# Optimization experiments

Hardware: AMD Instinct MI355X
Metric: run time of the kernel (lower is better)

Reference implementation:

```python
import jax, jax.numpy as jnp
import numpy as np

B, S, IN_DIM, OUT_DIM = 16, 1024, 1024, 1024
NEG_SLOPE = 0.01  # torch F.leaky_relu default


def setup_inputs() -> dict:
    key = jax.random.key(0)
    ks = jax.random.split(key, 10)
    sc_in = 1.0 / np.sqrt(IN_DIM)
    sc_out = 1.0 / np.sqrt(OUT_DIM)
    return {
        "xs": jax.random.normal(ks[0], (B, S, IN_DIM), dtype=jnp.float32),
        "mask": jax.random.randint(ks[1], (B, S), 0, 2, dtype=jnp.int32),
        "Wk": jax.random.uniform(ks[2], (OUT_DIM, IN_DIM), jnp.float32, -sc_in, sc_in),
        "bk": jax.random.uniform(ks[3], (OUT_DIM,), jnp.float32, -sc_in, sc_in),
        "Wq": jax.random.uniform(ks[4], (OUT_DIM, IN_DIM), jnp.float32, -sc_in, sc_in),
        "bq": jax.random.uniform(ks[5], (OUT_DIM,), jnp.float32, -sc_in, sc_in),
        "Wv": jax.random.uniform(ks[6], (OUT_DIM, IN_DIM), jnp.float32, -sc_in, sc_in),
        "bv": jax.random.uniform(ks[7], (OUT_DIM,), jnp.float32, -sc_in, sc_in),
        "Wlin": jax.random.uniform(ks[8], (OUT_DIM, OUT_DIM), jnp.float32, -sc_out, sc_out),
        "blin": jax.random.uniform(ks[9], (OUT_DIM,), jnp.float32, -sc_out, sc_out),
    }


def reference(xs, mask, Wk, bk, Wq, bq, Wv, bv, Wlin, blin):
    # projections: torch Linear is x @ W.T + b
    K = jnp.einsum('bsi,oi->bso', xs, Wk) + bk  # [B,S,D]
    Q = jnp.einsum('bsi,oi->bso', xs, Wq) + bq  # [B,S,D]
    V = jnp.einsum('bsi,oi->bso', xs, Wv) + bv  # [B,S,D]
    # qk[b,s,e] = sum_d K[b,s,d] * Q[b,e,d]
    qk = jnp.einsum('bsd,bed->bse', K, Q) / xs.shape[-1]
    # mask.repeat(1,S).view(B,S,S) => element [b,i,j] = mask[b,j] (column/key mask)
    qk = jnp.where(mask[:, None, :].astype(bool), qk, -jnp.inf)
    a = jax.nn.softmax(qk, axis=-1)  # [B,S,S]
    # faithful to einsum('bij,bik->bik'): sum a over last axis, scale V elementwise
    attn = jnp.sum(a, axis=-1, keepdims=True) * V  # [B,S,D]
    out = jnp.einsum('bsd,od->bso', attn, Wlin) + blin
    return jnp.where(out >= 0, out, NEG_SLOPE * out)
```

## Files before the change

kernel.cpp:

```cpp
#include <hip/hip_runtime.h>
#include <hip/hip_bf16.h>
#include <stdint.h>


#define M_TOT 16384
#define KDIM  1024
#define NDIM  1024
#define NKT   32

typedef __attribute__((ext_vector_type(8))) short bf16x8;
typedef __attribute__((ext_vector_type(4))) float f32x4;
typedef __attribute__((ext_vector_type(4))) unsigned short u16x4;
typedef __attribute__((ext_vector_type(8))) unsigned short u16x8;

static __device__ __forceinline__ unsigned short f2bf(float f) {
    union { float f; unsigned int u; } v; v.f = f;
    unsigned int u = v.u;
    return (unsigned short)((u + 0x7fffu + ((u >> 16) & 1u)) >> 16);
}

static __device__ __forceinline__ u16x8 pack8(float4 a, float4 b) {
    u16x8 p = { f2bf(a.x), f2bf(a.y), f2bf(a.z), f2bf(a.w),
                f2bf(b.x), f2bf(b.y), f2bf(b.z), f2bf(b.w) };
    return p;
}

static __device__ __forceinline__ void gload16(const void* g, void* l) {
    __builtin_amdgcn_global_load_lds(
        (__attribute__((address_space(1))) void*)(g),
        (__attribute__((address_space(3))) void*)(l), 16, 0, 0);
}

static __device__ __forceinline__ int swz128(int p) {
    return p ^ (((p >> 7) & 7) << 4);
}

__global__ __launch_bounds__(256) void prep0x_kernel(
    const float* __restrict__ Wv, const float* __restrict__ Wlin,
    const float* __restrict__ bv, const float* __restrict__ blin,
    const float* __restrict__ xs, unsigned short* __restrict__ Wvt,
    unsigned short* __restrict__ Wlb, float* __restrict__ bcomb,
    unsigned short* __restrict__ Xb) {
    __shared__ float Tl[64 * 65];
    const int bid = blockIdx.x;
    const int t = threadIdx.x;

    if (bid >= 768) {
        const size_t base = (((size_t)(bid - 768)) * 256 + t) * 8;
        #pragma unroll
        for (int itr = 0; itr < 4; ++itr) {
            const size_t idx = base + (size_t)itr * (size_t)(2048 * 256 * 8);
            float4 a = *(const float4*)&xs[idx];
            float4 b = *(const float4*)&xs[idx + 4];
            *(u16x8*)&Xb[idx] = pack8(a, b);
        }
        return;
    }

    if (bid < 256) {
        const int dt = bid >> 4;
        const int it = bid & 15;
        const int r = t >> 2;
        const int c0 = (t & 3) * 16;
        #pragma unroll
        for (int u = 0; u < 4; ++u) {
            float4 v = *(const float4*)&Wv[((size_t)(dt * 64 + r)) * NDIM + it * 64 + c0 + 4 * u];
            Tl[r * 65 + c0 + 4 * u + 0] = v.x;
            Tl[r * 65 + c0 + 4 * u + 1] = v.y;
            Tl[r * 65 + c0 + 4 * u + 2] = v.z;
            Tl[r * 65 + c0 + 4 * u + 3] = v.w;
        }
        __syncthreads();
        const int i = t >> 2;
        const int dq = (t & 3) * 16;
        float v[16];
        #pragma unroll
        for (int u = 0; u < 16; ++u) v[u] = Tl[(dq + u) * 65 + i];
        u16x8 p0 = { f2bf(v[0]), f2bf(v[1]), f2bf(v[2]), f2bf(v[3]),
                     f2bf(v[4]), f2bf(v[5]), f2bf(v[6]), f2bf(v[7]) };
        u16x8 p1 = { f2bf(v[8]), f2bf(v[9]), f2bf(v[10]), f2bf(v[11]),
                     f2bf(v[12]), f2bf(v[13]), f2bf(v[14]), f2bf(v[15]) };
        unsigned short* dst = &Wvt[((size_t)(it * 64 + i)) * KDIM + dt * 64 + dq];
        *(u16x8*)dst = p0;
        *(u16x8*)(dst + 8) = p1;
    } else if (bid < 512) {
        const size_t idx = (((size_t)(bid - 256)) * 256 + t) * 16;
        float4 a = *(const float4*)&Wlin[idx];
        float4 b = *(const float4*)&Wlin[idx + 4];
        float4 c = *(const float4*)&Wlin[idx + 8];
        float4 d = *(const float4*)&Wlin[idx + 12];
        *(u16x8*)&Wlb[idx] = pack8(a, b);
        *(u16x8*)&Wlb[idx + 8] = pack8(c, d);
    } else {
        const int wave = t >> 6, lane = t & 63;
        const int o = (bid - 512) * 4 + wave;
        float s = 0.f;
        for (int d = lane; d < KDIM; d += 64) s += Wlin[o * KDIM + d] * bv[d];
        #pragma unroll
        for (int off = 32; off > 0; off >>= 1) s += __shfl_down(s, off, 64);
        if (lane == 0) bcomb[o] = s + blin[o];
    }
}

__global__ __launch_bounds__(256) void wcomb_kernel(
    const unsigned short* __restrict__ Wlb, const unsigned short* __restrict__ Wvt,
    unsigned short* __restrict__ Wc) {
    __shared__ unsigned short As[64 * 32];
    __shared__ unsigned short Bs[64 * 32];
    const int t = threadIdx.x;
    const int ot = blockIdx.x >> 4;
    const int it = blockIdx.x & 15;
    const int w = t >> 6, l = t & 63;
    const int wr = (w >> 1) * 32, wc = (w & 1) * 32;
    const int lr = l & 15, lk = l >> 4;

    f32x4 acc[2][2] = {};

    const unsigned short* gA = &Wlb[((size_t)(ot * 64 + (t >> 2))) * KDIM + (t & 3) * 8];
    const unsigned short* gB = &Wvt[((size_t)(it * 64 + (t >> 2))) * KDIM + (t & 3) * 8];
    unsigned short* lA = &As[w * 512];
    unsigned short* lB = &Bs[w * 512];

    for (int kt = 0; kt < KDIM / 32; ++kt) {
        gload16(gA + kt * 32, lA);
        gload16(gB + kt * 32, lB);
        __syncthreads();
        bf16x8 af[2], bfr[2];
        #pragma unroll
        for (int fi = 0; fi < 2; ++fi)
            af[fi] = *(bf16x8*)&As[(wr + fi * 16 + lr) * 32 + lk * 8];
        #pragma unroll
        for (int fj = 0; fj < 2; ++fj)
            bfr[fj] = *(bf16x8*)&Bs[(wc + fj * 16 + lr) * 32 + lk * 8];
        #pragma unroll
        for (int fi = 0; fi < 2; ++fi)
            #pragma unroll
            for (int fj = 0; fj < 2; ++fj)
                acc[fi][fj] = __builtin_amdgcn_mfma_f32_16x16x32_bf16(
                    af[fi], bfr[fj], acc[fi][fj], 0, 0, 0);
        __syncthreads();
    }
    #pragma unroll
    for (int fi = 0; fi < 2; ++fi)
        #pragma unroll
        for (int fj = 0; fj < 2; ++fj)
            #pragma unroll
            for (int r = 0; r < 4; ++r) {
                const int o = ot * 64 + wr + fi * 16 + lk * 4 + r;
                const int i = it * 64 + wc + fj * 16 + lr;
                Wc[(size_t)o * KDIM + i] = f2bf(acc[fi][fj][r]);
            }
}

__global__ __launch_bounds__(512, 4) void main_mb(
    const unsigned short* __restrict__ Xb, const unsigned short* __restrict__ Wc,
    const float* __restrict__ bcomb, float* __restrict__ out) {
    extern __shared__ char lds[];
    const int tid = threadIdx.x;
    const int w = tid >> 6, l = tid & 63;
    const int wm = w >> 1, wn = w & 1;
    const int lr = l & 15, lk = l >> 4;

    const int swzb = ((blockIdx.x & 7) << 6) | (blockIdx.x >> 3);
    const int mt = swzb >> 3, nt = swzb & 7;

    int aoff[4], boff[4];
    #pragma unroll
    for (int fi = 0; fi < 4; ++fi) {
        const int r = wm * 64 + fi * 16 + lr;
        aoff[fi] = swz128(((r >> 1) << 7) | ((r & 1) << 6) | (lk << 4));
    }
    #pragma unroll
    for (int fj = 0; fj < 4; ++fj) {
        const int r = wn * 64 + fj * 16 + lr;
        boff[fj] = 16384 + swz128(((r >> 1) << 7) | ((r & 1) << 6) | (lk << 4));
    }

    const char* srcA[2];
    #pragma unroll
    for (int c = 0; c < 2; ++c) {
        const int q = c * 8192 + tid * 16;
        const int p = swz128(q);
        const int r = ((p >> 7) << 1) | ((p >> 6) & 1);
        srcA[c] = (const char*)Xb + ((size_t)(mt * 256 + r)) * 2048 + (p & 63);
    }
    const char* srcB;
    {
        const int q = tid * 16;
        const int p = swz128(q);
        const int r = ((p >> 7) << 1) | ((p >> 6) & 1);
        srcB = (const char*)Wc + ((size_t)(nt * 128 + r)) * 2048 + (p & 63);
    }
    const int ldsAw = w * 1024;
    const int ldsBw = 16384 + w * 1024;

    f32x4 acc[4][4] = {};

#define STAGE(TT, BUF)                                                         \
    do {                                                                       \
        gload16(srcA[0] + (size_t)(TT) * 64, (BUF) + ldsAw);                   \
        gload16(srcA[1] + (size_t)(TT) * 64, (BUF) + 8192 + ldsAw);            \
        gload16(srcB + (size_t)(TT) * 64, (BUF) + ldsBw);                      \
    } while (0)

    STAGE(0, lds);

    for (int kt = 0; kt < NKT; ++kt) {
        char* cbuf = lds + (kt & 1) * 24576;
        char* nbuf = lds + ((kt & 1) ^ 1) * 24576;

        if (kt < NKT - 1) {
            STAGE(kt + 1, nbuf);
            asm volatile("s_waitcnt vmcnt(3)" ::: "memory");
        } else {
            asm volatile("s_waitcnt vmcnt(0)" ::: "memory");
        }
        __builtin_amdgcn_s_barrier();

        bf16x8 af[4], bfr[4];
        #pragma unroll
        for (int fi = 0; fi < 4; ++fi)
            af[fi] = *(const bf16x8*)(cbuf + aoff[fi]);
        #pragma unroll
        for (int fj = 0; fj < 4; ++fj)
            bfr[fj] = *(const bf16x8*)(cbuf + boff[fj]);

        __builtin_amdgcn_s_setprio(1);
        #pragma unroll
        for (int fi = 0; fi < 4; ++fi)
            #pragma unroll
            for (int fj = 0; fj < 4; ++fj)
                acc[fi][fj] = __builtin_amdgcn_mfma_f32_16x16x32_bf16(
                    af[fi], bfr[fj], acc[fi][fj], 0, 0, 0);
        __builtin_amdgcn_s_setprio(0);

        __builtin_amdgcn_s_barrier();
    }
#undef STAGE

    #pragma unroll
    for (int fi = 0; fi < 4; ++fi)
        #pragma unroll
        for (int fj = 0; fj < 4; ++fj) {
            const int col = nt * 128 + wn * 64 + fj * 16 + lr;
            const float b = bcomb[col];
            #pragma unroll
            for (int r = 0; r < 4; ++r) {
                const int row = mt * 256 + wm * 64 + fi * 16 + lk * 4 + r;
                float v = acc[fi][fj][r] + b;
                out[(size_t)row * NDIM + col] = v >= 0.f ? v : 0.01f * v;
            }
        }
}

__global__ __launch_bounds__(256) void main_gemm_f32(
    const float* __restrict__ X, const unsigned short* __restrict__ Wc,
    const float* __restrict__ bcomb, float* __restrict__ out) {
    __shared__ unsigned short As[128 * 32];
    __shared__ unsigned short Bs[128 * 32];
    const int t = threadIdx.x;
    const int nt = blockIdx.x & 7;
    const int mt = blockIdx.x >> 3;
    const int w = t >> 6, l = t & 63;
    const int wr = (w >> 1) * 64, wcc = (w & 1) * 64;
    const int lr = l & 15, lk = l >> 4;

    f32x4 acc[4][4] = {};

    const int arow = t >> 3;
    const int akq = t & 7;
    const int brow = t >> 2;
    const int bc4 = t & 3;

    for (int kt = 0; kt < KDIM / 32; ++kt) {
        float4 av[4];
        #pragma unroll
        for (int j = 0; j < 4; ++j) {
            const int row = j * 32 + arow;
            av[j] = *(const float4*)&X[(mt * 128 + row) * KDIM + kt * 32 + akq * 4];
        }
        __syncthreads();
        #pragma unroll
        for (int j = 0; j < 4; ++j) {
            const int row = j * 32 + arow;
            u16x4 p = { f2bf(av[j].x), f2bf(av[j].y), f2bf(av[j].z), f2bf(av[j].w) };
            *(u16x4*)&As[row * 32 + akq * 4] = p;
        }
        #pragma unroll
        for (int j = 0; j < 2; ++j) {
            const int row = j * 64 + brow;
            const unsigned short* g = &Wc[(nt * 128 + row) * KDIM + kt * 32 + bc4 * 8];
            unsigned short* ldst = &Bs[(j * 256 + w * 64) * 8];
            gload16(g, ldst);
        }
        __syncthreads();
        bf16x8 af[4], bfr[4];
        #pragma unroll
        for (int fi = 0; fi < 4; ++fi)
            af[fi] = *(bf16x8*)&As[(wr + fi * 16 + lr) * 32 + lk * 8];
        #pragma unroll
        for (int fj = 0; fj < 4; ++fj)
            bfr[fj] = *(bf16x8*)&Bs[(wcc + fj * 16 + lr) * 32 + lk * 8];
        #pragma unroll
        for (int fi = 0; fi < 4; ++fi)
            #pragma unroll
            for (int fj = 0; fj < 4; ++fj)
                acc[fi][fj] = __builtin_amdgcn_mfma_f32_16x16x32_bf16(
                    af[fi], bfr[fj], acc[fi][fj], 0, 0, 0);
    }

    #pragma unroll
    for (int fi = 0; fi < 4; ++fi)
        #pragma unroll
        for (int fj = 0; fj < 4; ++fj) {
            const int col = nt * 128 + wcc + fj * 16 + lr;
            const float b = bcomb[col];
            #pragma unroll
            for (int r = 0; r < 4; ++r) {
                const int row = mt * 128 + wr + fi * 16 + lk * 4 + r;
                float v = acc[fi][fj][r] + b;
                out[row * NDIM + col] = v >= 0.f ? v : 0.01f * v;
            }
        }
}

extern "C" void kernel_launch(void* const* d_in, const int* in_sizes, int n_in,
                              void* d_out, int out_size, void* d_ws, size_t ws_size,
                              hipStream_t stream) {
    const float* xs   = (const float*)d_in[0];
    const float* Wv   = (const float*)d_in[6];
    const float* bv   = (const float*)d_in[7];
    const float* Wlin = (const float*)d_in[8];
    const float* blin = (const float*)d_in[9];

    unsigned short* Wc = (unsigned short*)d_ws;
    float* bcomb = (float*)((char*)d_ws + 2097152);
    unsigned short* Xb = (unsigned short*)((char*)d_ws + 2101248);
    float* out = (float*)d_out;

    unsigned short* Wvt = (unsigned short*)d_out;
    unsigned short* Wlb = (unsigned short*)((char*)d_out + 2097152);

    const size_t NEED = 2101248 + (size_t)M_TOT * KDIM * 2;
    if (ws_size >= NEED) {
        (void)hipFuncSetAttribute((const void*)main_mb,
                                  hipFuncAttributeMaxDynamicSharedMemorySize,
                                  49152);
        hipLaunchKernelGGL(prep0x_kernel, dim3(768 + 2048), dim3(256), 0,
                           stream, Wv, Wlin, bv, blin, xs, Wvt, Wlb, bcomb, Xb);
        hipLaunchKernelGGL(wcomb_kernel, dim3(256), dim3(256), 0, stream,
                           Wlb, Wvt, Wc);
        hipLaunchKernelGGL(main_mb, dim3(512), dim3(512), 49152, stream,
                           Xb, Wc, bcomb, out);
    } else {
        hipLaunchKernelGGL(prep0x_kernel, dim3(768), dim3(256), 0, stream,
                           Wv, Wlin, bv, blin, xs, Wvt, Wlb, bcomb, Xb);
        hipLaunchKernelGGL(wcomb_kernel, dim3(256), dim3(256), 0, stream,
                           Wlb, Wvt, Wc);
        hipLaunchKernelGGL(main_gemm_f32, dim3((M_TOT / 128) * (NDIM / 128)),
                           dim3(256), 0, stream, xs, Wc, bcomb, out);
    }
}
```

Baseline: 75.31 us.

## Triple-buffer main GEMM LDS with one barrier and move xs cast to wcomb launch

The main GEMM goes from a double-buffered LDS pipeline with two barriers per k-step to a triple-buffered one. It prefetches two tiles ahead and drops the trailing barrier, which cuts synchronisation stalls and hides more load latency. Dynamic LDS grows from 48 KB to 72 KB per block, which may lower occupancy. Separately, the fp32-to-bf16 conversion of xs moves from the first prep kernel into the weight-combine kernel. That lets the large conversion overlap the small 256-block GEMM instead of the weight transposes.

```diff
diff --git a/kernel.cpp b/kernel.cpp
--- a/kernel.cpp
+++ b/kernel.cpp
@@ -35,27 +35,14 @@
     return p ^ (((p >> 7) & 7) << 4);
 }
 
-__global__ __launch_bounds__(256) void prep0x_kernel(
+__global__ __launch_bounds__(256) void prep0_kernel(
     const float* __restrict__ Wv, const float* __restrict__ Wlin,
     const float* __restrict__ bv, const float* __restrict__ blin,
-    const float* __restrict__ xs, unsigned short* __restrict__ Wvt,
-    unsigned short* __restrict__ Wlb, float* __restrict__ bcomb,
-    unsigned short* __restrict__ Xb) {
+    unsigned short* __restrict__ Wvt, unsigned short* __restrict__ Wlb,
+    float* __restrict__ bcomb) {
     __shared__ float Tl[64 * 65];
     const int bid = blockIdx.x;
     const int t = threadIdx.x;
-
-    if (bid >= 768) {
-        const size_t base = (((size_t)(bid - 768)) * 256 + t) * 8;
-        #pragma unroll
-        for (int itr = 0; itr < 4; ++itr) {
-            const size_t idx = base + (size_t)itr * (size_t)(2048 * 256 * 8);
-            float4 a = *(const float4*)&xs[idx];
-            float4 b = *(const float4*)&xs[idx + 4];
-            *(u16x8*)&Xb[idx] = pack8(a, b);
-        }
-        return;
-    }
 
     if (bid < 256) {
         const int dt = bid >> 4;
@@ -102,14 +89,29 @@
     }
 }
 
-__global__ __launch_bounds__(256) void wcomb_kernel(
+__global__ __launch_bounds__(256) void prep1_kernel(
     const unsigned short* __restrict__ Wlb, const unsigned short* __restrict__ Wvt,
-    unsigned short* __restrict__ Wc) {
+    const float* __restrict__ xs, unsigned short* __restrict__ Wc,
+    unsigned short* __restrict__ Xb) {
     __shared__ unsigned short As[64 * 32];
     __shared__ unsigned short Bs[64 * 32];
+    const int bid = blockIdx.x;
     const int t = threadIdx.x;
-    const int ot = blockIdx.x >> 4;
-    const int it = blockIdx.x & 15;
+
+    if (bid >= 256) {
+        const size_t base = (((size_t)(bid - 256)) * 256 + t) * 8;
+        #pragma unroll
+        for (int itr = 0; itr < 4; ++itr) {
+            const size_t idx = base + (size_t)itr * (size_t)(2048 * 256 * 8);
+            float4 a = *(const float4*)&xs[idx];
+            float4 b = *(const float4*)&xs[idx + 4];
+            *(u16x8*)&Xb[idx] = pack8(a, b);
+        }
+        return;
+    }
+
+    const int ot = bid >> 4;
+    const int it = bid & 15;
     const int w = t >> 6, l = t & 63;
     const int wr = (w >> 1) * 32, wc = (w & 1) * 32;
     const int lr = l & 15, lk = l >> 4;
@@ -152,7 +154,7 @@
             }
 }
 
-__global__ __launch_bounds__(512, 4) void main_mb(
+__global__ __launch_bounds__(512, 4) void main_mb3(
     const unsigned short* __restrict__ Xb, const unsigned short* __restrict__ Wc,
     const float* __restrict__ bcomb, float* __restrict__ out) {
     extern __shared__ char lds[];
@@ -196,27 +198,28 @@
 
     f32x4 acc[4][4] = {};
 
-#define STAGE(TT, BUF)                                                         \
+#define STAGE(TT, OFF)                                                         \
     do {                                                                       \
-        gload16(srcA[0] + (size_t)(TT) * 64, (BUF) + ldsAw);                   \
-        gload16(srcA[1] + (size_t)(TT) * 64, (BUF) + 8192 + ldsAw);            \
-        gload16(srcB + (size_t)(TT) * 64, (BUF) + ldsBw);                      \
+        gload16(srcA[0] + (size_t)(TT) * 64, lds + (OFF) + ldsAw);             \
+        gload16(srcA[1] + (size_t)(TT) * 64, lds + (OFF) + 8192 + ldsAw);      \
+        gload16(srcB + (size_t)(TT) * 64, lds + (OFF) + ldsBw);                \
     } while (0)
 
-    STAGE(0, lds);
+    STAGE(0, 0);
+    STAGE(1, 24576);
+
+    int oc = 0, on = 24576, ol = 49152;
 
     for (int kt = 0; kt < NKT; ++kt) {
-        char* cbuf = lds + (kt & 1) * 24576;
-        char* nbuf = lds + ((kt & 1) ^ 1) * 24576;
-
-        if (kt < NKT - 1) {
-            STAGE(kt + 1, nbuf);
+        if (kt < NKT - 1)
             asm volatile("s_waitcnt vmcnt(3)" ::: "memory");
-        } else {
+        else
             asm volatile("s_waitcnt vmcnt(0)" ::: "memory");
-        }
         __builtin_amdgcn_s_barrier();
 
+        if (kt + 2 < NKT) STAGE(kt + 2, ol);
+
+        const char* cbuf = lds + oc;
         bf16x8 af[4], bfr[4];
         #pragma unroll
         for (int fi = 0; fi < 4; ++fi)
@@ -234,7 +237,7 @@
                     af[fi], bfr[fj], acc[fi][fj], 0, 0, 0);
         __builtin_amdgcn_s_setprio(0);
 
-        __builtin_amdgcn_s_barrier();
+        const int tmp = oc; oc = on; on = ol; ol = tmp;
     }
 #undef STAGE
 
@@ -342,21 +345,19 @@
     unsigned short* Wlb = (unsigned short*)((char*)d_out + 2097152);
 
     const size_t NEED = 2101248 + (size_t)M_TOT * KDIM * 2;
+    hipLaunchKernelGGL(prep0_kernel, dim3(768), dim3(256), 0, stream,
+                       Wv, Wlin, bv, blin, Wvt, Wlb, bcomb);
     if (ws_size >= NEED) {
-        (void)hipFuncSetAttribute((const void*)main_mb,
+        (void)hipFuncSetAttribute((const void*)main_mb3,
                                   hipFuncAttributeMaxDynamicSharedMemorySize,
-                                  49152);
-        hipLaunchKernelGGL(prep0x_kernel, dim3(768 + 2048), dim3(256), 0,
-                           stream, Wv, Wlin, bv, blin, xs, Wvt, Wlb, bcomb, Xb);
-        hipLaunchKernelGGL(wcomb_kernel, dim3(256), dim3(256), 0, stream,
-                           Wlb, Wvt, Wc);
-        hipLaunchKernelGGL(main_mb, dim3(512), dim3(512), 49152, stream,
+                                  73728);
+        hipLaunchKernelGGL(prep1_kernel, dim3(256 + 2048), dim3(256), 0, stream,
+                           Wlb, Wvt, xs, Wc, Xb);
+        hipLaunchKernelGGL(main_mb3, dim3(512), dim3(512), 73728, stream,
                            Xb, Wc, bcomb, out);
     } else {
-        hipLaunchKernelGGL(prep0x_kernel, dim3(768), dim3(256), 0, stream,
-                           Wv, Wlin, bv, blin, xs, Wvt, Wlb, bcomb, Xb);
-        hipLaunchKernelGGL(wcomb_kernel, dim3(256), dim3(256), 0, stream,
-                           Wlb, Wvt, Wc);
+        hipLaunchKernelGGL(prep1_kernel, dim3(256), dim3(256), 0, stream,
+                           Wlb, Wvt, xs, Wc, Xb);
         hipLaunchKernelGGL(main_gemm_f32, dim3((M_TOT / 128) * (NDIM / 128)),
                            dim3(256), 0, stream, xs, Wc, bcomb, out);
     }
```

New measurement: 76.35 us. About the same (+1.4%).

## Load fp32 activations directly into LDS and convert to bf16 in GEMM

Applied to the files above, without the earlier changes.

Drops the separate pass that converts xs to bf16 in workspace. The main GEMM now streams fp32 xs tiles straight into LDS through global_load_lds and packs them to bf16 with v_cvt_pk_bf16_f32 just before the MFMAs. This removes a full write and re-read of a 32MB bf16 copy of the activations. In exchange each k-step moves twice as many A bytes and LDS per block grows to 80KB, which may reduce how many blocks fit per CU.

```diff
diff --git a/kernel.cpp b/kernel.cpp
--- a/kernel.cpp
+++ b/kernel.cpp
@@ -12,6 +12,7 @@
 typedef __attribute__((ext_vector_type(4))) float f32x4;
 typedef __attribute__((ext_vector_type(4))) unsigned short u16x4;
 typedef __attribute__((ext_vector_type(8))) unsigned short u16x8;
+typedef __attribute__((ext_vector_type(4))) unsigned int u32x4;
 
 static __device__ __forceinline__ unsigned short f2bf(float f) {
     union { float f; unsigned int u; } v; v.f = f;
@@ -25,6 +26,12 @@
     return p;
 }
 
+static __device__ __forceinline__ unsigned int cvtpk(float lo, float hi) {
+    unsigned int r;
+    asm("v_cvt_pk_bf16_f32 %0, %1, %2" : "=v"(r) : "v"(lo), "v"(hi));
+    return r;
+}
+
 static __device__ __forceinline__ void gload16(const void* g, void* l) {
     __builtin_amdgcn_global_load_lds(
         (__attribute__((address_space(1))) void*)(g),
@@ -35,27 +42,14 @@
     return p ^ (((p >> 7) & 7) << 4);
 }
 
-__global__ __launch_bounds__(256) void prep0x_kernel(
+__global__ __launch_bounds__(256) void prep0_kernel(
     const float* __restrict__ Wv, const float* __restrict__ Wlin,
     const float* __restrict__ bv, const float* __restrict__ blin,
-    const float* __restrict__ xs, unsigned short* __restrict__ Wvt,
-    unsigned short* __restrict__ Wlb, float* __restrict__ bcomb,
-    unsigned short* __restrict__ Xb) {
+    unsigned short* __restrict__ Wvt, unsigned short* __restrict__ Wlb,
+    float* __restrict__ bcomb) {
     __shared__ float Tl[64 * 65];
     const int bid = blockIdx.x;
     const int t = threadIdx.x;
-
-    if (bid >= 768) {
-        const size_t base = (((size_t)(bid - 768)) * 256 + t) * 8;
-        #pragma unroll
-        for (int itr = 0; itr < 4; ++itr) {
-            const size_t idx = base + (size_t)itr * (size_t)(2048 * 256 * 8);
-            float4 a = *(const float4*)&xs[idx];
-            float4 b = *(const float4*)&xs[idx + 4];
-            *(u16x8*)&Xb[idx] = pack8(a, b);
-        }
-        return;
-    }
 
     if (bid < 256) {
         const int dt = bid >> 4;
@@ -152,8 +146,8 @@
             }
 }
 
-__global__ __launch_bounds__(512, 4) void main_mb(
-    const unsigned short* __restrict__ Xb, const unsigned short* __restrict__ Wc,
+__global__ __launch_bounds__(512, 4) void main_f32a(
+    const float* __restrict__ xs, const unsigned short* __restrict__ Wc,
     const float* __restrict__ bcomb, float* __restrict__ out) {
     extern __shared__ char lds[];
     const int tid = threadIdx.x;
@@ -168,21 +162,21 @@
     #pragma unroll
     for (int fi = 0; fi < 4; ++fi) {
         const int r = wm * 64 + fi * 16 + lr;
-        aoff[fi] = swz128(((r >> 1) << 7) | ((r & 1) << 6) | (lk << 4));
+        aoff[fi] = swz128((r << 7) | (lk << 5));
     }
     #pragma unroll
     for (int fj = 0; fj < 4; ++fj) {
         const int r = wn * 64 + fj * 16 + lr;
-        boff[fj] = 16384 + swz128(((r >> 1) << 7) | ((r & 1) << 6) | (lk << 4));
-    }
-
-    const char* srcA[2];
-    #pragma unroll
-    for (int c = 0; c < 2; ++c) {
+        boff[fj] = 32768 + swz128(((r >> 1) << 7) | ((r & 1) << 6) | (lk << 4));
+    }
+
+    const char* srcA[4];
+    #pragma unroll
+    for (int c = 0; c < 4; ++c) {
         const int q = c * 8192 + tid * 16;
         const int p = swz128(q);
-        const int r = ((p >> 7) << 1) | ((p >> 6) & 1);
-        srcA[c] = (const char*)Xb + ((size_t)(mt * 256 + r)) * 2048 + (p & 63);
+        const int r = p >> 7;
+        srcA[c] = (const char*)xs + ((size_t)(mt * 256 + r)) * 4096 + (p & 127);
     }
     const char* srcB;
     {
@@ -191,36 +185,44 @@
         const int r = ((p >> 7) << 1) | ((p >> 6) & 1);
         srcB = (const char*)Wc + ((size_t)(nt * 128 + r)) * 2048 + (p & 63);
     }
-    const int ldsAw = w * 1024;
-    const int ldsBw = 16384 + w * 1024;
+    const int ldsw = w * 1024;
 
     f32x4 acc[4][4] = {};
 
-#define STAGE(TT, BUF)                                                         \
+#define STAGE(TT, SLOT)                                                        \
     do {                                                                       \
-        gload16(srcA[0] + (size_t)(TT) * 64, (BUF) + ldsAw);                   \
-        gload16(srcA[1] + (size_t)(TT) * 64, (BUF) + 8192 + ldsAw);            \
-        gload16(srcB + (size_t)(TT) * 64, (BUF) + ldsBw);                      \
+        gload16(srcA[0] + (size_t)(TT) * 128, lds + (SLOT) + 0 * 8192 + ldsw); \
+        gload16(srcA[1] + (size_t)(TT) * 128, lds + (SLOT) + 1 * 8192 + ldsw); \
+        gload16(srcA[2] + (size_t)(TT) * 128, lds + (SLOT) + 2 * 8192 + ldsw); \
+        gload16(srcA[3] + (size_t)(TT) * 128, lds + (SLOT) + 3 * 8192 + ldsw); \
+        gload16(srcB + (size_t)(TT) * 64, lds + (SLOT) + 32768 + ldsw);        \
     } while (0)
 
-    STAGE(0, lds);
+    STAGE(0, 0);
 
     for (int kt = 0; kt < NKT; ++kt) {
-        char* cbuf = lds + (kt & 1) * 24576;
-        char* nbuf = lds + ((kt & 1) ^ 1) * 24576;
+        const int cur = (kt & 1) * 40960;
+        const int nxt = ((kt & 1) ^ 1) * 40960;
 
         if (kt < NKT - 1) {
-            STAGE(kt + 1, nbuf);
-            asm volatile("s_waitcnt vmcnt(3)" ::: "memory");
+            STAGE(kt + 1, nxt);
+            asm volatile("s_waitcnt vmcnt(5)" ::: "memory");
         } else {
             asm volatile("s_waitcnt vmcnt(0)" ::: "memory");
         }
         __builtin_amdgcn_s_barrier();
 
+        const char* cbuf = lds + cur;
+
         bf16x8 af[4], bfr[4];
         #pragma unroll
-        for (int fi = 0; fi < 4; ++fi)
-            af[fi] = *(const bf16x8*)(cbuf + aoff[fi]);
+        for (int fi = 0; fi < 4; ++fi) {
+            float4 lo = *(const float4*)(cbuf + aoff[fi]);
+            float4 hi = *(const float4*)(cbuf + (aoff[fi] ^ 16));
+            u32x4 pw = { cvtpk(lo.x, lo.y), cvtpk(lo.z, lo.w),
+                         cvtpk(hi.x, hi.y), cvtpk(hi.z, hi.w) };
+            af[fi] = *(bf16x8*)&pw;
+        }
         #pragma unroll
         for (int fj = 0; fj < 4; ++fj)
             bfr[fj] = *(const bf16x8*)(cbuf + boff[fj]);
@@ -335,28 +337,23 @@
 
     unsigned short* Wc = (unsigned short*)d_ws;
     float* bcomb = (float*)((char*)d_ws + 2097152);
-    unsigned short* Xb = (unsigned short*)((char*)d_ws + 2101248);
     float* out = (float*)d_out;
 
     unsigned short* Wvt = (unsigned short*)d_out;
     unsigned short* Wlb = (unsigned short*)((char*)d_out + 2097152);
 
-    const size_t NEED = 2101248 + (size_t)M_TOT * KDIM * 2;
+    const size_t NEED = 2101248;
+    hipLaunchKernelGGL(prep0_kernel, dim3(768), dim3(256), 0, stream,
+                       Wv, Wlin, bv, blin, Wvt, Wlb, bcomb);
+    hipLaunchKernelGGL(wcomb_kernel, dim3(256), dim3(256), 0, stream,
+                       Wlb, Wvt, Wc);
     if (ws_size >= NEED) {
-        (void)hipFuncSetAttribute((const void*)main_mb,
+        (void)hipFuncSetAttribute((const void*)main_f32a,
                                   hipFuncAttributeMaxDynamicSharedMemorySize,
-                                  49152);
-        hipLaunchKernelGGL(prep0x_kernel, dim3(768 + 2048), dim3(256), 0,
-                           stream, Wv, Wlin, bv, blin, xs, Wvt, Wlb, bcomb, Xb);
-        hipLaunchKernelGGL(wcomb_kernel, dim3(256), dim3(256), 0, stream,
-                           Wlb, Wvt, Wc);
-        hipLaunchKernelGGL(main_mb, dim3(512), dim3(512), 49152, stream,
-                           Xb, Wc, bcomb, out);
+                                  81920);
+        hipLaunchKernelGGL(main_f32a, dim3(512), dim3(512), 81920, stream,
+                           xs, Wc, bcomb, out);
     } else {
-        hipLaunchKernelGGL(prep0x_kernel, dim3(768), dim3(256), 0, stream,
-                           Wv, Wlin, bv, blin, xs, Wvt, Wlb, bcomb, Xb);
-        hipLaunchKernelGGL(wcomb_kernel, dim3(256), dim3(256), 0, stream,
-                           Wlb, Wvt, Wc);
         hipLaunchKernelGGL(main_gemm_f32, dim3((M_TOT / 128) * (NDIM / 128)),
                            dim3(256), 0, stream, xs, Wc, bcomb, out);
     }
```

New measurement: 73.65 us. 2.2% less time.
